# Kernel tuning notes

Measured on AMD Instinct MI355X. Metric: run time of the kernel, lower is better.

The kernel has to match this reference:

```python
import jax, jax.numpy as jnp
import numpy as np

N = 100000      # num nodes
E = 1600000     # num edges
F_IN = 128      # feature_dim
H = 128         # hidden_channels
B = 8192        # num link queries


def setup_inputs() -> dict:
    key = jax.random.key(0)
    ks = jax.random.split(key, 13)
    x = jax.random.normal(ks[0], (N, F_IN), dtype=jnp.float32)
    edge_index = jax.random.randint(ks[1], (2, E), 0, N, dtype=jnp.int32)
    root_n_index = jax.random.randint(ks[2], (B, 2), 0, N, dtype=jnp.int32)
    s = 1.0 / np.sqrt(H).astype(np.float32)
    W1 = jax.random.normal(ks[3], (F_IN, H), jnp.float32) * s
    b1 = jnp.zeros((H,), jnp.float32)
    W2 = jax.random.normal(ks[4], (H, H), jnp.float32) * s
    b2 = jnp.zeros((H,), jnp.float32)
    W3 = jax.random.normal(ks[5], (H, H), jnp.float32) * s
    b3 = jnp.zeros((H,), jnp.float32)
    P1 = jax.random.normal(ks[6], (H, H), jnp.float32) * s
    pb1 = jnp.zeros((H,), jnp.float32)
    P2 = jax.random.normal(ks[7], (H, 1), jnp.float32) * s
    pb2 = jnp.zeros((1,), jnp.float32)
    return {"x": x, "edge_index": edge_index, "root_n_index": root_n_index,
            "W1": W1, "b1": b1, "W2": W2, "b2": b2, "W3": W3, "b3": b3,
            "P1": P1, "pb1": pb1, "P2": P2, "pb2": pb2}


def gcn_conv(h, src, dst, norm, W, b):
    # transform then gather-scale-scatter: out = D^-1/2 (A+I) D^-1/2 (h W) + b
    h = h @ W                                  # [N, H]
    msg = h[src] * norm[:, None]               # [E+N, H]
    return jax.ops.segment_sum(msg, dst, num_segments=N) + b


def reference(x, edge_index, root_n_index, W1, b1, W2, b2, W3, b3, P1, pb1, P2, pb2):
    # add self loops (GCNConv default) and compute symmetric normalization once
    loop = jnp.arange(N, dtype=edge_index.dtype)
    src = jnp.concatenate([edge_index[0], loop])
    dst = jnp.concatenate([edge_index[1], loop])
    deg = jax.ops.segment_sum(jnp.ones_like(dst, jnp.float32), dst, num_segments=N)
    dinv = jnp.where(deg > 0, jax.lax.rsqrt(jnp.maximum(deg, 1.0)), 0.0)
    norm = dinv[src] * dinv[dst]

    # 3 stacked GCN layers; dropout is identity in eval mode
    h = jax.nn.relu(gcn_conv(x, src, dst, norm, W1, b1))
    h = jax.nn.relu(gcn_conv(h, src, dst, norm, W2, b2))
    h = gcn_conv(h, src, dst, norm, W3, b3)

    # link embeddings: elementwise product of src/dst node embeddings
    link = h[root_n_index[:, 0]] * h[root_n_index[:, 1]]   # [B, H]
    link = jax.nn.relu(link @ P1 + pb1)
    logits = (link @ P2 + pb2).squeeze(-1)                 # [B]
    return logits
```

## Files before the change

kernel.cpp:

```cpp
#include <hip/hip_runtime.h>

#define NN 100000
#define EE 1600000
#define HH 128
#define BB 8192
#define SCAN_NBLK ((NN + 1023) / 1024)


__global__ void hist_kernel(const int* __restrict__ dst, int* __restrict__ hist) {
    int e = blockIdx.x * blockDim.x + threadIdx.x;
    if (e < EE) atomicAdd(&hist[dst[e]], 1);
}

__global__ void dinv_kernel(const int* __restrict__ hist, float* __restrict__ dinv) {
    int i = blockIdx.x * blockDim.x + threadIdx.x;
    if (i < NN) dinv[i] = rsqrtf((float)hist[i] + 1.0f);
}


__global__ __launch_bounds__(1024) void scan_partial_kernel(const int* __restrict__ hist,
        int* __restrict__ bsum) {
    __shared__ int red[1024];
    int i = blockIdx.x * 1024 + threadIdx.x;
    int v = (i < NN) ? hist[i] : 0;
    red[threadIdx.x] = v;
    __syncthreads();
    for (int d = 512; d > 0; d >>= 1) {
        if (threadIdx.x < d) red[threadIdx.x] += red[threadIdx.x + d];
        __syncthreads();
    }
    if (threadIdx.x == 0) bsum[blockIdx.x] = red[0];
}

__global__ void scan_sums_kernel(const int* __restrict__ bsum, int* __restrict__ bbase) {
    int acc = 0;
    for (int b = 0; b < SCAN_NBLK; ++b) { bbase[b] = acc; acc += bsum[b]; }
    bbase[SCAN_NBLK] = acc;
}

__global__ __launch_bounds__(1024) void scan_offs_kernel(const int* __restrict__ hist,
        const int* __restrict__ bbase, int* __restrict__ offs, int* __restrict__ cursor) {
    __shared__ int sc[1024];
    int i = blockIdx.x * 1024 + threadIdx.x;
    int v = (i < NN) ? hist[i] : 0;
    sc[threadIdx.x] = v;
    __syncthreads();
    for (int d = 1; d < 1024; d <<= 1) {
        int t = (threadIdx.x >= d) ? sc[threadIdx.x - d] : 0;
        __syncthreads();
        sc[threadIdx.x] += t;
        __syncthreads();
    }
    if (i < NN) {
        int excl = bbase[blockIdx.x] + sc[threadIdx.x] - v;
        offs[i] = excl;
        cursor[i] = excl;
        if (i == NN - 1) offs[NN] = excl + v;
    }
}

__global__ void fill_kernel(const int* __restrict__ src, const int* __restrict__ dst,
        const float* __restrict__ dinv, int* __restrict__ cursor,
        int* __restrict__ esrc, float* __restrict__ enorm) {
    int e = blockIdx.x * blockDim.x + threadIdx.x;
    if (e >= EE) return;
    int s = src[e], d = dst[e];
    int p = atomicAdd(&cursor[d], 1);
    esrc[p] = s;
    enorm[p] = dinv[s] * dinv[d];
}


__global__ __launch_bounds__(256) void gemm128(const float* __restrict__ A,
        const float* __restrict__ W, const float* __restrict__ bias,
        float* __restrict__ C, int M, int relu) {
    __shared__ float Ws[64 * 128];
    __shared__ float As[64 * 64];
    const int tid = threadIdx.x;
    const int row0 = blockIdx.x * 64;
    const int tcol = tid & 31, trow = tid >> 5;

    float acc[8][4];
#pragma unroll
    for (int r = 0; r < 8; ++r)
#pragma unroll
        for (int i = 0; i < 4; ++i) acc[r][i] = 0.f;

    for (int kc = 0; kc < 128; kc += 64) {
        __syncthreads();
#pragma unroll
        for (int i = 0; i < 8; ++i) {
            int p = tid + 256 * i;
            ((float4*)Ws)[p] = ((const float4*)W)[kc * 32 + p];
        }
#pragma unroll
        for (int i = 0; i < 4; ++i) {
            int p = tid + 256 * i;
            int r = p >> 4, c4 = p & 15;
            int gr = row0 + r;
            float4 v = make_float4(0.f, 0.f, 0.f, 0.f);
            if (gr < M) v = *(const float4*)&A[(size_t)gr * HH + kc + c4 * 4];
            ((float4*)As)[p] = v;
        }
        __syncthreads();

#pragma unroll
        for (int k4 = 0; k4 < 16; ++k4) {
            float4 a[8];
#pragma unroll
            for (int r = 0; r < 8; ++r)
                a[r] = *(const float4*)&As[(trow * 8 + r) * 64 + k4 * 4];
#pragma unroll
            for (int j = 0; j < 4; ++j) {
                float w[4];
#pragma unroll
                for (int i = 0; i < 4; ++i)
                    w[i] = Ws[(k4 * 4 + j) * 128 + tcol + 32 * i];
#pragma unroll
                for (int r = 0; r < 8; ++r) {
                    float av = (j == 0) ? a[r].x : (j == 1) ? a[r].y : (j == 2) ? a[r].z : a[r].w;
#pragma unroll
                    for (int i = 0; i < 4; ++i) acc[r][i] += av * w[i];
                }
            }
        }
    }

    float bv[4] = {0.f, 0.f, 0.f, 0.f};
    if (bias) {
#pragma unroll
        for (int i = 0; i < 4; ++i) bv[i] = bias[tcol + 32 * i];
    }
#pragma unroll
    for (int r = 0; r < 8; ++r) {
        int gr = row0 + trow * 8 + r;
        if (gr < M) {
#pragma unroll
            for (int i = 0; i < 4; ++i) {
                float v = acc[r][i] + bv[i];
                if (relu) v = fmaxf(v, 0.f);
                C[(size_t)gr * HH + tcol + 32 * i] = v;
            }
        }
    }
}


__global__ __launch_bounds__(256) void agg_kernel(const float* __restrict__ t,
        float* __restrict__ out, const int* __restrict__ offs,
        const int* __restrict__ esrc, const float* __restrict__ enorm,
        const float* __restrict__ dinv, const float* __restrict__ bias, int relu) {
    const int wave = threadIdx.x >> 6;
    const int lane = threadIdx.x & 63;
    const int node = blockIdx.x * 4 + wave;
    if (node >= NN) return;
    const int f = lane * 2;

    float di = dinv[node];
    float2 sv = *(const float2*)&t[(size_t)node * HH + f];
    float ax = sv.x * di * di;
    float ay = sv.y * di * di;

    int e = offs[node];
    const int e1 = offs[node + 1];
    for (; e + 4 <= e1; e += 4) {
        int s0 = esrc[e], s1 = esrc[e + 1], s2 = esrc[e + 2], s3 = esrc[e + 3];
        float n0 = enorm[e], n1 = enorm[e + 1], n2 = enorm[e + 2], n3 = enorm[e + 3];
        float2 v0 = *(const float2*)&t[(size_t)s0 * HH + f];
        float2 v1 = *(const float2*)&t[(size_t)s1 * HH + f];
        float2 v2 = *(const float2*)&t[(size_t)s2 * HH + f];
        float2 v3 = *(const float2*)&t[(size_t)s3 * HH + f];
        ax += v0.x * n0; ay += v0.y * n0;
        ax += v1.x * n1; ay += v1.y * n1;
        ax += v2.x * n2; ay += v2.y * n2;
        ax += v3.x * n3; ay += v3.y * n3;
    }
    for (; e < e1; ++e) {
        int s = esrc[e];
        float nm = enorm[e];
        float2 v = *(const float2*)&t[(size_t)s * HH + f];
        ax += v.x * nm; ay += v.y * nm;
    }

    float2 b = make_float2(0.f, 0.f);
    if (bias) b = *(const float2*)&bias[f];
    ax += b.x; ay += b.y;
    if (relu) { ax = fmaxf(ax, 0.f); ay = fmaxf(ay, 0.f); }
    *(float2*)&out[(size_t)node * HH + f] = make_float2(ax, ay);
}


__global__ __launch_bounds__(256) void link_kernel(const float* __restrict__ h,
        const int* __restrict__ roots, float* __restrict__ linkb) {
    const int wave = threadIdx.x >> 6;
    const int lane = threadIdx.x & 63;
    const int b = blockIdx.x * 4 + wave;
    if (b >= BB) return;
    const int f = lane * 2;
    int r0 = roots[b * 2], r1 = roots[b * 2 + 1];
    float2 u = *(const float2*)&h[(size_t)r0 * HH + f];
    float2 v = *(const float2*)&h[(size_t)r1 * HH + f];
    *(float2*)&linkb[(size_t)b * HH + f] = make_float2(u.x * v.x, u.y * v.y);
}

__global__ __launch_bounds__(256) void logits_kernel(const float* __restrict__ g,
        const float* __restrict__ P2, const float* __restrict__ pb2,
        float* __restrict__ out) {
    const int wave = threadIdx.x >> 6;
    const int lane = threadIdx.x & 63;
    const int b = blockIdx.x * 4 + wave;
    if (b >= BB) return;
    const int f = lane * 2;
    float2 gv = *(const float2*)&g[(size_t)b * HH + f];
    float2 pv = *(const float2*)&P2[f];
    float s = gv.x * pv.x + gv.y * pv.y;
    for (int off = 32; off > 0; off >>= 1) s += __shfl_down(s, off);
    if (lane == 0) out[b] = s + pb2[0];
}


extern "C" void kernel_launch(void* const* d_in, const int* in_sizes, int n_in,
                              void* d_out, int out_size, void* d_ws, size_t ws_size,
                              hipStream_t stream) {
    const float* x   = (const float*)d_in[0];
    const int*   ei  = (const int*)d_in[1];
    const int* roots = (const int*)d_in[2];
    const float* W1  = (const float*)d_in[3];
    const float* b1  = (const float*)d_in[4];
    const float* W2  = (const float*)d_in[5];
    const float* b2  = (const float*)d_in[6];
    const float* W3  = (const float*)d_in[7];
    const float* b3  = (const float*)d_in[8];
    const float* P1  = (const float*)d_in[9];
    const float* pb1 = (const float*)d_in[10];
    const float* P2  = (const float*)d_in[11];
    const float* pb2 = (const float*)d_in[12];
    float* out = (float*)d_out;
    (void)in_sizes; (void)n_in; (void)out_size; (void)ws_size;

    char* ws = (char*)d_ws;
    size_t woff = 0;
    auto alloc = [&](size_t bytes) {
        void* p = ws + woff;
        woff += (bytes + 255) & ~(size_t)255;
        return p;
    };
    int*   hist   = (int*)  alloc((size_t)NN * 4);
    float* dinv   = (float*)alloc((size_t)NN * 4);
    int*   offs   = (int*)  alloc((size_t)(NN + 1) * 4);
    int*   cursor = (int*)  alloc((size_t)NN * 4);
    int*   bsum   = (int*)  alloc((size_t)(SCAN_NBLK + 1) * 4);
    int*   bbase  = (int*)  alloc((size_t)(SCAN_NBLK + 1) * 4);
    int*   esrc   = (int*)  alloc((size_t)EE * 4);
    float* enorm  = (float*)alloc((size_t)EE * 4);
    float* bufA   = (float*)alloc((size_t)NN * HH * 4);
    float* bufB   = (float*)alloc((size_t)NN * HH * 4);
    float* linkb  = (float*)alloc((size_t)BB * HH * 4);
    float* gout   = (float*)alloc((size_t)BB * HH * 4);

    const int* e_src = ei;
    const int* e_dst = ei + EE;

    hipMemsetAsync(hist, 0, (size_t)NN * 4, stream);
    hist_kernel<<<(EE + 255) / 256, 256, 0, stream>>>(e_dst, hist);
    dinv_kernel<<<(NN + 255) / 256, 256, 0, stream>>>(hist, dinv);
    scan_partial_kernel<<<SCAN_NBLK, 1024, 0, stream>>>(hist, bsum);
    scan_sums_kernel<<<1, 1, 0, stream>>>(bsum, bbase);
    scan_offs_kernel<<<SCAN_NBLK, 1024, 0, stream>>>(hist, bbase, offs, cursor);
    fill_kernel<<<(EE + 255) / 256, 256, 0, stream>>>(e_src, e_dst, dinv, cursor, esrc, enorm);

    gemm128<<<(NN + 63) / 64, 256, 0, stream>>>(x, W1, nullptr, bufA, NN, 0);
    agg_kernel<<<(NN + 3) / 4, 256, 0, stream>>>(bufA, bufB, offs, esrc, enorm, dinv, b1, 1);
    gemm128<<<(NN + 63) / 64, 256, 0, stream>>>(bufB, W2, nullptr, bufA, NN, 0);
    agg_kernel<<<(NN + 3) / 4, 256, 0, stream>>>(bufA, bufB, offs, esrc, enorm, dinv, b2, 1);
    gemm128<<<(NN + 63) / 64, 256, 0, stream>>>(bufB, W3, nullptr, bufA, NN, 0);
    agg_kernel<<<(NN + 3) / 4, 256, 0, stream>>>(bufA, bufB, offs, esrc, enorm, dinv, b3, 0);

    link_kernel<<<(BB + 3) / 4, 256, 0, stream>>>(bufB, roots, linkb);
    gemm128<<<(BB + 63) / 64, 256, 0, stream>>>(linkb, P1, pb1, gout, BB, 1);
    logits_kernel<<<(BB + 3) / 4, 256, 0, stream>>>(gout, P2, pb2, out);
}
```

Baseline: 852.8 us.

## Enlarge GEMM tile to 128x128 and split edges across half-waves in aggregation

New measurement: 896.2 us. +5.1%, slower.

```diff
diff --git a/kernel.cpp b/kernel.cpp
--- a/kernel.cpp
+++ b/kernel.cpp
@@ -16,7 +16,6 @@
     int i = blockIdx.x * blockDim.x + threadIdx.x;
     if (i < NN) dinv[i] = rsqrtf((float)hist[i] + 1.0f);
 }
-
 
 __global__ __launch_bounds__(1024) void scan_partial_kernel(const int* __restrict__ hist,
         int* __restrict__ bsum) {
@@ -74,33 +73,37 @@
 __global__ __launch_bounds__(256) void gemm128(const float* __restrict__ A,
         const float* __restrict__ W, const float* __restrict__ bias,
         float* __restrict__ C, int M, int relu) {
-    __shared__ float Ws[64 * 128];
-    __shared__ float As[64 * 64];
+    __shared__ float4 As4[16 * 128];
+    __shared__ float4 Ws4[64 * 32];
     const int tid = threadIdx.x;
-    const int row0 = blockIdx.x * 64;
-    const int tcol = tid & 31, trow = tid >> 5;
-
-    float acc[8][4];
+    const int row0 = blockIdx.x * 128;
+    const int tcol8 = tid & 15;
+    const int trowg = tid >> 4;
+
+    float acc[8][8];
 #pragma unroll
     for (int r = 0; r < 8; ++r)
 #pragma unroll
-        for (int i = 0; i < 4; ++i) acc[r][i] = 0.f;
+        for (int c = 0; c < 8; ++c) acc[r][c] = 0.f;
+
+    const float4* A4 = (const float4*)A;
+    const float4* W4 = (const float4*)W;
 
     for (int kc = 0; kc < 128; kc += 64) {
         __syncthreads();
 #pragma unroll
         for (int i = 0; i < 8; ++i) {
             int p = tid + 256 * i;
-            ((float4*)Ws)[p] = ((const float4*)W)[kc * 32 + p];
-        }
-#pragma unroll
-        for (int i = 0; i < 4; ++i) {
+            int row = p >> 4, k4 = p & 15;
+            int gr = row0 + row;
+            float4 v = make_float4(0.f, 0.f, 0.f, 0.f);
+            if (gr < M) v = A4[(size_t)gr * 32 + (kc >> 2) + k4];
+            As4[k4 * 128 + row] = v;
+        }
+#pragma unroll
+        for (int i = 0; i < 8; ++i) {
             int p = tid + 256 * i;
-            int r = p >> 4, c4 = p & 15;
-            int gr = row0 + r;
-            float4 v = make_float4(0.f, 0.f, 0.f, 0.f);
-            if (gr < M) v = *(const float4*)&A[(size_t)gr * HH + kc + c4 * 4];
-            ((float4*)As)[p] = v;
+            Ws4[p] = W4[(size_t)kc * 32 + p];
         }
         __syncthreads();
 
@@ -109,38 +112,47 @@
             float4 a[8];
 #pragma unroll
             for (int r = 0; r < 8; ++r)
-                a[r] = *(const float4*)&As[(trow * 8 + r) * 64 + k4 * 4];
-#pragma unroll
-            for (int j = 0; j < 4; ++j) {
-                float w[4];
-#pragma unroll
-                for (int i = 0; i < 4; ++i)
-                    w[i] = Ws[(k4 * 4 + j) * 128 + tcol + 32 * i];
+                a[r] = As4[k4 * 128 + trowg + 16 * r];
+#pragma unroll
+            for (int kk = 0; kk < 4; ++kk) {
+                int k = k4 * 4 + kk;
+                float4 w0 = Ws4[k * 32 + tcol8 * 2];
+                float4 w1 = Ws4[k * 32 + tcol8 * 2 + 1];
 #pragma unroll
                 for (int r = 0; r < 8; ++r) {
-                    float av = (j == 0) ? a[r].x : (j == 1) ? a[r].y : (j == 2) ? a[r].z : a[r].w;
-#pragma unroll
-                    for (int i = 0; i < 4; ++i) acc[r][i] += av * w[i];
+                    float av = (kk == 0) ? a[r].x : (kk == 1) ? a[r].y
+                             : (kk == 2) ? a[r].z : a[r].w;
+                    acc[r][0] += av * w0.x; acc[r][1] += av * w0.y;
+                    acc[r][2] += av * w0.z; acc[r][3] += av * w0.w;
+                    acc[r][4] += av * w1.x; acc[r][5] += av * w1.y;
+                    acc[r][6] += av * w1.z; acc[r][7] += av * w1.w;
                 }
             }
         }
     }
 
-    float bv[4] = {0.f, 0.f, 0.f, 0.f};
+    float bv[8];
+#pragma unroll
+    for (int c = 0; c < 8; ++c) bv[c] = 0.f;
     if (bias) {
-#pragma unroll
-        for (int i = 0; i < 4; ++i) bv[i] = bias[tcol + 32 * i];
-    }
+        float4 b0 = ((const float4*)bias)[tcol8 * 2];
+        float4 b1 = ((const float4*)bias)[tcol8 * 2 + 1];
+        bv[0] = b0.x; bv[1] = b0.y; bv[2] = b0.z; bv[3] = b0.w;
+        bv[4] = b1.x; bv[5] = b1.y; bv[6] = b1.z; bv[7] = b1.w;
+    }
+    float4* C4 = (float4*)C;
 #pragma unroll
     for (int r = 0; r < 8; ++r) {
-        int gr = row0 + trow * 8 + r;
+        int gr = row0 + trowg + 16 * r;
         if (gr < M) {
-#pragma unroll
-            for (int i = 0; i < 4; ++i) {
-                float v = acc[r][i] + bv[i];
-                if (relu) v = fmaxf(v, 0.f);
-                C[(size_t)gr * HH + tcol + 32 * i] = v;
+            float o[8];
+#pragma unroll
+            for (int c = 0; c < 8; ++c) {
+                float v = acc[r][c] + bv[c];
+                o[c] = relu ? fmaxf(v, 0.f) : v;
             }
+            C4[(size_t)gr * 32 + tcol8 * 2]     = make_float4(o[0], o[1], o[2], o[3]);
+            C4[(size_t)gr * 32 + tcol8 * 2 + 1] = make_float4(o[4], o[5], o[6], o[7]);
         }
     }
 }
@@ -154,39 +166,63 @@
     const int lane = threadIdx.x & 63;
     const int node = blockIdx.x * 4 + wave;
     if (node >= NN) return;
-    const int f = lane * 2;
-
-    float di = dinv[node];
-    float2 sv = *(const float2*)&t[(size_t)node * HH + f];
-    float ax = sv.x * di * di;
-    float ay = sv.y * di * di;
+    const int half = lane >> 5;
+    const int hl = lane & 31;
+
+    const float4* t4 = (const float4*)t;
+    float ax = 0.f, ay = 0.f, az = 0.f, aw = 0.f;
+
+    if (half == 0) {
+        float di = dinv[node];
+        float s = di * di;
+        float4 sv = t4[(size_t)node * 32 + hl];
+        ax = sv.x * s; ay = sv.y * s; az = sv.z * s; aw = sv.w * s;
+    }
 
     int e = offs[node];
     const int e1 = offs[node + 1];
-    for (; e + 4 <= e1; e += 4) {
-        int s0 = esrc[e], s1 = esrc[e + 1], s2 = esrc[e + 2], s3 = esrc[e + 3];
-        float n0 = enorm[e], n1 = enorm[e + 1], n2 = enorm[e + 2], n3 = enorm[e + 3];
-        float2 v0 = *(const float2*)&t[(size_t)s0 * HH + f];
-        float2 v1 = *(const float2*)&t[(size_t)s1 * HH + f];
-        float2 v2 = *(const float2*)&t[(size_t)s2 * HH + f];
-        float2 v3 = *(const float2*)&t[(size_t)s3 * HH + f];
-        ax += v0.x * n0; ay += v0.y * n0;
-        ax += v1.x * n1; ay += v1.y * n1;
-        ax += v2.x * n2; ay += v2.y * n2;
-        ax += v3.x * n3; ay += v3.y * n3;
-    }
-    for (; e < e1; ++e) {
+    for (; e + 8 <= e1; e += 8) {
+        int i0 = e + half,     i1 = e + 2 + half;
+        int i2 = e + 4 + half, i3 = e + 6 + half;
+        int s0 = esrc[i0], s1 = esrc[i1], s2 = esrc[i2], s3 = esrc[i3];
+        float n0 = enorm[i0], n1 = enorm[i1], n2 = enorm[i2], n3 = enorm[i3];
+        float4 v0 = t4[(size_t)s0 * 32 + hl];
+        float4 v1 = t4[(size_t)s1 * 32 + hl];
+        float4 v2 = t4[(size_t)s2 * 32 + hl];
+        float4 v3 = t4[(size_t)s3 * 32 + hl];
+        ax += v0.x * n0; ay += v0.y * n0; az += v0.z * n0; aw += v0.w * n0;
+        ax += v1.x * n1; ay += v1.y * n1; az += v1.z * n1; aw += v1.w * n1;
+        ax += v2.x * n2; ay += v2.y * n2; az += v2.z * n2; aw += v2.w * n2;
+        ax += v3.x * n3; ay += v3.y * n3; az += v3.z * n3; aw += v3.w * n3;
+    }
+    for (; e + 2 <= e1; e += 2) {
+        int ee = e + half;
+        int s = esrc[ee];
+        float nm = enorm[ee];
+        float4 v = t4[(size_t)s * 32 + hl];
+        ax += v.x * nm; ay += v.y * nm; az += v.z * nm; aw += v.w * nm;
+    }
+    if (e < e1 && half == 0) {
         int s = esrc[e];
         float nm = enorm[e];
-        float2 v = *(const float2*)&t[(size_t)s * HH + f];
-        ax += v.x * nm; ay += v.y * nm;
-    }
-
-    float2 b = make_float2(0.f, 0.f);
-    if (bias) b = *(const float2*)&bias[f];
-    ax += b.x; ay += b.y;
-    if (relu) { ax = fmaxf(ax, 0.f); ay = fmaxf(ay, 0.f); }
-    *(float2*)&out[(size_t)node * HH + f] = make_float2(ax, ay);
+        float4 v = t4[(size_t)s * 32 + hl];
+        ax += v.x * nm; ay += v.y * nm; az += v.z * nm; aw += v.w * nm;
+    }
+
+    ax += __shfl_xor(ax, 32); ay += __shfl_xor(ay, 32);
+    az += __shfl_xor(az, 32); aw += __shfl_xor(aw, 32);
+
+    if (half == 0) {
+        if (bias) {
+            float4 b = ((const float4*)bias)[hl];
+            ax += b.x; ay += b.y; az += b.z; aw += b.w;
+        }
+        if (relu) {
+            ax = fmaxf(ax, 0.f); ay = fmaxf(ay, 0.f);
+            az = fmaxf(az, 0.f); aw = fmaxf(aw, 0.f);
+        }
+        ((float4*)out)[(size_t)node * 32 + hl] = make_float4(ax, ay, az, aw);
+    }
 }
 
 
@@ -269,14 +305,14 @@
     scan_offs_kernel<<<SCAN_NBLK, 1024, 0, stream>>>(hist, bbase, offs, cursor);
     fill_kernel<<<(EE + 255) / 256, 256, 0, stream>>>(e_src, e_dst, dinv, cursor, esrc, enorm);
 
-    gemm128<<<(NN + 63) / 64, 256, 0, stream>>>(x, W1, nullptr, bufA, NN, 0);
+    gemm128<<<(NN + 127) / 128, 256, 0, stream>>>(x, W1, nullptr, bufA, NN, 0);
     agg_kernel<<<(NN + 3) / 4, 256, 0, stream>>>(bufA, bufB, offs, esrc, enorm, dinv, b1, 1);
-    gemm128<<<(NN + 63) / 64, 256, 0, stream>>>(bufB, W2, nullptr, bufA, NN, 0);
+    gemm128<<<(NN + 127) / 128, 256, 0, stream>>>(bufB, W2, nullptr, bufA, NN, 0);
     agg_kernel<<<(NN + 3) / 4, 256, 0, stream>>>(bufA, bufB, offs, esrc, enorm, dinv, b2, 1);
-    gemm128<<<(NN + 63) / 64, 256, 0, stream>>>(bufB, W3, nullptr, bufA, NN, 0);
+    gemm128<<<(NN + 127) / 128, 256, 0, stream>>>(bufB, W3, nullptr, bufA, NN, 0);
     agg_kernel<<<(NN + 3) / 4, 256, 0, stream>>>(bufA, bufB, offs, esrc, enorm, dinv, b3, 0);
 
     link_kernel<<<(BB + 3) / 4, 256, 0, stream>>>(bufB, roots, linkb);
-    gemm128<<<(BB + 63) / 64, 256, 0, stream>>>(linkb, P1, pb1, gout, BB, 1);
+    gemm128<<<(BB + 127) / 128, 256, 0, stream>>>(linkb, P1, pb1, gout, BB, 1);
     logits_kernel<<<(BB + 3) / 4, 256, 0, stream>>>(gout, P2, pb2, out);
 }
```
